# Kernel optimization log

Hardware: AMD Instinct MI355X
Metric: run time of the kernel (lower is better)

Reference implementation:

```python
import jax, jax.numpy as jnp
import numpy as np

T = 1_000_000          # number of t_eval points (~1 year at 30 s)
N_ROOMS = 10
N = 12                 # 2 latent wall nodes + n_rooms
DT = 30.0              # seconds between t_eval points
LOAD_SCALE = 50.0      # physical_cooling_scaling: W/m^2 scale for sigmoid(loads)


def setup_inputs() -> dict:
    key = jax.random.key(0)
    k1, k2, k3, k4, k5 = jax.random.split(key, 5)
    t_eval = jnp.arange(T, dtype=jnp.float32) * DT
    x0 = 26.0 * jnp.ones((N,), jnp.float32)  # reset_iv: 26 C at every node
    # Stable slow RC dynamics: negative-definite-ish A with small coupling
    A = (-1e-5 * jnp.eye(N, dtype=jnp.float32)
         + 1e-6 * jax.random.normal(k1, (N, N), jnp.float32))
    B = 1e-6 * jax.random.normal(k2, (N, 1 + N_ROOMS), jnp.float32)
    Tout_data = 10.0 + 20.0 * jax.random.uniform(k3, (T,), jnp.float32)  # outdoor temp samples on t_eval grid
    loads_raw = jax.random.normal(k4, (2, N_ROOMS), jnp.float32)         # pre-sigmoid [cool; gain] loads
    room_areas = 10.0 + 40.0 * jax.random.uniform(k5, (N_ROOMS,), jnp.float32)
    return {"t_eval": t_eval, "x0": x0, "A": A, "B": B,
            "Tout_data": Tout_data, "loads_raw": loads_raw, "room_areas": room_areas}


def reference(t_eval, x0, A, B, Tout_data, loads_raw, room_areas):
    # transform + physical scaling of loads (self.transform = sigmoid)
    loads = jax.nn.sigmoid(loads_raw) * LOAD_SCALE
    cool_load, gain_load = loads[0], loads[1]
    action = 0.0  # no cooling policy -> self.action stays 0
    Q_area = -cool_load * action + gain_load            # [n_rooms]
    Q_watts = Q_area * room_areas                        # proportional_heating
    # u = [Tout; Q_watts] so B@u = B[:,0]*Tout + B[:,1:]@Q_watts (Q constant over t)
    b0 = B[:, 0]                                         # [N]
    Bq = B[:, 1:] @ Q_watts                              # [N], constant forcing
    h = t_eval[1] - t_eval[0]                            # uniform step
    # Linear interp of Tout: value at t_i, midpoint t_i+h/2, and t_{i+1}
    To_t = Tout_data[:-1]
    To_n = Tout_data[1:]
    To_m = 0.5 * (To_t + To_n)

    def f(x, To):  # dy/dt = A x + B u
        return A @ x + b0 * To + Bq

    def step(x, tou):
        to_t, to_m, to_n = tou
        k1 = f(x, to_t)
        k2 = f(x + 0.5 * h * k1, to_m)
        k3 = f(x + 0.5 * h * k2, to_m)
        k4 = f(x + h * k3, to_n)
        xn = x + (h / 6.0) * (k1 + 2.0 * k2 + 2.0 * k3 + k4)
        return xn, xn

    _, xs = jax.lax.scan(step, x0, (To_t, To_m, To_n))
    return jnp.concatenate([x0[None, :], xs], axis=0)  # [T, N]
```

## Files before the change

kernel.cpp:

```cpp
#include <hip/hip_runtime.h>
#include <math.h>


#define S_STEPS 999999
#define CH      8
#define BLK     256
#define NB      489
#define NCHUNK  125000
#define LASTFULL 124998

#define OFF_M   0
#define OFF_C   144
#define OFF_AL  156
#define OFF_BE  168
#define OFF_K   192
#define OFF_P2  320
#define OFF_PA  1472
#define OFF_PL  1616
#define OFF_PD  2048
#define OFF_AGG 3200

#define FMA4(Q,a,b,c,d,acc) fmaf((Q).w,(d),fmaf((Q).z,(c),fmaf((Q).y,(b),fmaf((Q).x,(a),(acc)))))

__device__ __forceinline__ void mv_acc(const float* Pf, const float* x, float* y) {
  const float4* P = reinterpret_cast<const float4*>(Pf);
#pragma unroll
  for (int i = 0; i < 12; ++i) {
    float4 a = P[3*i], b = P[3*i+1], c = P[3*i+2];
    y[i] = FMA4(c, x[8],x[9],x[10],x[11],
            FMA4(b, x[4],x[5],x[6],x[7],
             FMA4(a, x[0],x[1],x[2],x[3], y[i])));
  }
}

__device__ __forceinline__ float rowdot(const float* Prow, const float* xv) {
  const float4* P = reinterpret_cast<const float4*>(Prow);
  float4 a = P[0], b = P[1], c = P[2];
  return FMA4(c, xv[8],xv[9],xv[10],xv[11],
          FMA4(b, xv[4],xv[5],xv[6],xv[7],
           FMA4(a, xv[0],xv[1],xv[2],xv[3], 0.f)));
}

__device__ __forceinline__ void fold_chunk(const float* __restrict__ cons,
                                           const float* tos, float* v) {
  const float4* Kq = reinterpret_cast<const float4*>(cons + OFF_K);
  float4 c0=Kq[0], c1=Kq[1], c2=Kq[2];
  v[0]=c0.x; v[1]=c0.y; v[2]=c0.z; v[3]=c0.w;
  v[4]=c1.x; v[5]=c1.y; v[6]=c1.z; v[7]=c1.w;
  v[8]=c2.x; v[9]=c2.y; v[10]=c2.z; v[11]=c2.w;
#pragma unroll
  for (int s = 0; s < 9; ++s) {
    float ts = tos[s];
    float4 ka=Kq[3*(s+1)], kb=Kq[3*(s+1)+1], kc=Kq[3*(s+1)+2];
    v[0]=fmaf(ka.x,ts,v[0]); v[1]=fmaf(ka.y,ts,v[1]); v[2]=fmaf(ka.z,ts,v[2]); v[3]=fmaf(ka.w,ts,v[3]);
    v[4]=fmaf(kb.x,ts,v[4]); v[5]=fmaf(kb.y,ts,v[5]); v[6]=fmaf(kb.z,ts,v[6]); v[7]=fmaf(kb.w,ts,v[7]);
    v[8]=fmaf(kc.x,ts,v[8]); v[9]=fmaf(kc.y,ts,v[9]); v[10]=fmaf(kc.z,ts,v[10]); v[11]=fmaf(kc.w,ts,v[11]);
  }
}

__global__ void __launch_bounds__(512) setup_kernel(
    const float* __restrict__ t_eval, const float* __restrict__ A,
    const float* __restrict__ Bm, const float* __restrict__ loads_raw,
    const float* __restrict__ areas, float* ws) {
  __shared__ double H1[144], H2[144], H3[144], H4[144], Md[144];
  __shared__ double Qa[144], Qb[144];
  __shared__ double C512s[144], C1024s[144], C2048s[144], C4096s[144];
  __shared__ double C8192s[144], C16384s[144], C32768s[144], Pd3s[144];
  __shared__ double cd[12], ald[12], bed[12], b0d[12], bqd[12];
  __shared__ double Vv[3][12], Kd[120];
  int t = threadIdx.x;
  double h = (double)t_eval[1] - (double)t_eval[0];
  if (t < 144) H1[t] = h * (double)A[t];
  if (t < 12) {
    b0d[t] = (double)Bm[t*11];
    double s = 0.0;
    for (int r = 0; r < 10; ++r) {
      double gq = 50.0 / (1.0 + exp(-(double)loads_raw[10 + r]));
      s += (double)Bm[t*11 + 1 + r] * (gq * (double)areas[r]);
    }
    bqd[t] = s;
  }
  if (t < 120) Kd[t] = 0.0;
  __syncthreads();
  if (t < 144) {
    int i=t/12, j=t%12; double s=0.0;
#pragma unroll
    for (int m = 0; m < 12; ++m) s += H1[i*12+m]*H1[m*12+j];
    H2[t]=s;
  }
  __syncthreads();
  if (t < 288) {
    int w=t/144, e=t%144, i=e/12, j=e%12;
    const double* Bp = w ? H2 : H1;
    double s = 0.0;
#pragma unroll
    for (int m = 0; m < 12; ++m) s += H2[i*12+m]*Bp[m*12+j];
    (w ? H4 : H3)[e] = s;
  }
  __syncthreads();
  if (t < 12) {
    double hb=0,h2b=0,h3b=0,hb0=0,h2b0=0,h3b0=0;
#pragma unroll
    for (int m = 0; m < 12; ++m) {
      hb  += H1[t*12+m]*bqd[m]; h2b  += H2[t*12+m]*bqd[m]; h3b  += H3[t*12+m]*bqd[m];
      hb0 += H1[t*12+m]*b0d[m]; h2b0 += H2[t*12+m]*b0d[m]; h3b0 += H3[t*12+m]*b0d[m];
    }
    double h6 = h / 6.0;
    cd[t]  = h6*(6.0*bqd[t] + 3.0*hb + h2b + 0.25*h3b);
    ald[t] = h6*(3.0*b0d[t] + 2.0*hb0 + 0.75*h2b0 + 0.25*h3b0);
    bed[t] = h6*(3.0*b0d[t] + hb0 + 0.25*h2b0);
    Vv[0][t]=ald[t]; Vv[1][t]=bed[t]; Vv[2][t]=cd[t];
    Kd[96+t] += ald[t]; Kd[108+t] += bed[t]; Kd[t] += cd[t];
  }
  if (t >= 144 && t < 288) {
    int e=t-144, i=e/12, j=e%12;
    Md[e] = (i==j ? 1.0 : 0.0) + H1[e] + 0.5*H2[e] + H3[e]/6.0 + H4[e]/24.0;
  }
  __syncthreads();
  if (t < 144) { ws[OFF_M+t] = (float)Md[t]; Qa[t] = Md[t]; }
  if (t < 12) {
    ws[OFF_C+t]=(float)cd[t]; ws[OFF_AL+t]=(float)ald[t]; ws[OFF_BE+t]=(float)bed[t];
  }
  __syncthreads();
  double* src = Qa; double* dst = Qb;
  for (int r = 1; r <= 15; ++r) {
    double acc = 0.0, ks = 0.0;
    if (t < 144) {
      int i=t/12, j=t%12;
#pragma unroll
      for (int m = 0; m < 12; ++m) acc += src[i*12+m]*src[m*12+j];
    }
    int w=0, i2=0;
    if (r <= 7 && t >= 256 && t < 292) {
      w=(t-256)/12; i2=(t-256)%12;
#pragma unroll
      for (int m = 0; m < 12; ++m) ks += Md[i2*12+m]*Vv[w][m];
    }
    __syncthreads();
    if (t < 144) {
      dst[t] = acc;
      if (r >= 3 && r <= 10) ws[OFF_P2+(r-3)*144+t] = (float)acc;
      if (r == 9)  C512s[t]=acc;
      if (r == 10) C1024s[t]=acc;
      if (r == 11) { C2048s[t]=acc;  ws[OFF_PL+t]       = (float)acc; }
      if (r == 12) { C4096s[t]=acc;  ws[OFF_PL+144+t]   = (float)acc; }
      if (r == 13) { C8192s[t]=acc;  ws[OFF_PD+144+t]   = (float)acc; }
      if (r == 14) { C16384s[t]=acc; ws[OFF_PD+2*144+t] = (float)acc; }
      if (r == 15) { C32768s[t]=acc; ws[OFF_PD+4*144+t] = (float)acc; }
    }
    if (r <= 7 && t >= 256 && t < 292) {
      Vv[w][i2] = ks;
      if (w == 0) Kd[(8-r)*12+i2] += ks;
      else if (w == 1) Kd[(9-r)*12+i2] += ks;
      else Kd[i2] += ks;
    }
    __syncthreads();
    double* tmp = src; src = dst; dst = tmp;
  }
  if (t < 120) ws[OFF_K+t] = (float)Kd[t];
  if (t < 144) ws[OFF_PD+t] = (t % 13 == 0) ? 1.f : 0.f;
  if (t < 432) {
    int w=t/144, e=t%144, i=e/12, j=e%12;
    const double* Ap = (w==0) ? C512s  : ((w==1) ? C2048s : C8192s);
    const double* Bp = (w==0) ? C1024s : ((w==1) ? C4096s : C16384s);
    double s = 0.0;
#pragma unroll
    for (int m = 0; m < 12; ++m) s += Ap[i*12+m]*Bp[m*12+j];
    if (w==0) ws[OFF_PA+e] = (float)s;
    else if (w==1) ws[OFF_PL+2*144+e] = (float)s;
    else { ws[OFF_PD+3*144+e] = (float)s; Pd3s[e] = s; }
  }
  __syncthreads();
  if (t < 432) {
    int w=t/144, e=t%144, i=e/12, j=e%12;
    const double* Ap = (w==0) ? C8192s : ((w==1) ? C16384s : Pd3s);
    double s = 0.0;
#pragma unroll
    for (int m = 0; m < 12; ++m) s += Ap[i*12+m]*C32768s[m*12+j];
    ws[OFF_PD+(5+w)*144+e] = (float)s;
  }
}

__global__ void __launch_bounds__(BLK, 2) block_agg(
    const float* __restrict__ cons, const float* __restrict__ To,
    const float* __restrict__ x0, float* __restrict__ agg) {
  __shared__ __align__(16) float Tw[48], Ta[24];
  int k = threadIdx.x, b = blockIdx.x;
  int g = b*BLK + k, base = g*CH;
  bool fullc = (g <= LASTFULL);
  float to_[9];
#pragma unroll
  for (int i = 0; i < 9; ++i) to_[i] = 0.f;
  if (fullc) {
    const float4* tp = reinterpret_cast<const float4*>(To + base);
    float4 ta = tp[0], tb = tp[1];
    to_[0]=ta.x; to_[1]=ta.y; to_[2]=ta.z; to_[3]=ta.w;
    to_[4]=tb.x; to_[5]=tb.y; to_[6]=tb.z; to_[7]=tb.w;
    to_[8]=To[base+8];
  }
  float v[12];
  if (fullc) fold_chunk(cons, to_, v);
  else {
#pragma unroll
    for (int i = 0; i < 12; ++i) v[i] = 0.f;
  }
  if (g == 0) {
    float xi[12];
#pragma unroll
    for (int i = 0; i < 12; ++i) xi[i] = x0[i];
    mv_acc(cons + OFF_P2, xi, v);
  }
  int j = k & 63;
#pragma unroll
  for (int l = 0; l < 6; ++l) {
    int off = 1 << l;
    float nb[12];
#pragma unroll
    for (int i = 0; i < 12; ++i) nb[i] = __shfl_up(v[i], (unsigned)off, 64);
    if (j >= off) mv_acc(cons + OFF_P2 + l*144, nb, v);
  }
  if (j == 63) {
#pragma unroll
    for (int i = 0; i < 12; ++i) Tw[(k>>6)*12 + i] = v[i];
  }
  __syncthreads();
  if (k < 24) {
    int p = k/12, comp = k - p*12;
    Ta[k] = rowdot(cons + OFF_P2 + 6*144 + comp*12, Tw + 2*p*12)
          + Tw[(2*p+1)*12 + comp];
  }
  __syncthreads();
  if (k < 12) {
    agg[b*12 + k] = rowdot(cons + OFF_P2 + 7*144 + k*12, Ta) + Ta[12 + k];
  }
}

__global__ void __launch_bounds__(BLK, 2) scan_expand(
    const float* __restrict__ cons, const float* __restrict__ To,
    const float* __restrict__ x0, const float* __restrict__ agg,
    float* __restrict__ out) {
  __shared__ __align__(16) float Tw[48];
  __shared__ __align__(16) float Pw[48];
  __shared__ __align__(16) float lkb[32*12];
  __shared__ __align__(16) float yv[8*12];
  __shared__ __align__(16) float zv[8*12];
  __shared__ __align__(16) float Xs[12];
  __shared__ __align__(16) float Qw[48];
  int k = threadIdx.x, b = blockIdx.x;
  int g = b*BLK + k, base = g*CH;
  bool active = (g < NCHUNK), fullc = (g <= LASTFULL);
  float to_[9];
#pragma unroll
  for (int i = 0; i < 9; ++i) to_[i] = 0.f;
  if (active) {
    const float4* tp = reinterpret_cast<const float4*>(To + base);
    float4 ta = tp[0], tb = tp[1];
    to_[0]=ta.x; to_[1]=ta.y; to_[2]=ta.z; to_[3]=ta.w;
    to_[4]=tb.x; to_[5]=tb.y; to_[6]=tb.z; to_[7]=tb.w;
    to_[8] = fullc ? To[base+8] : 0.f;
  }
  float v[12];
  if (fullc) fold_chunk(cons, to_, v);
  else {
#pragma unroll
    for (int i = 0; i < 12; ++i) v[i] = 0.f;
  }
  if (g == 0) {
    float xi[12];
#pragma unroll
    for (int i = 0; i < 12; ++i) xi[i] = x0[i];
    mv_acc(cons + OFF_P2, xi, v);
  }
  int j = k & 63, w = k >> 6;
#pragma unroll
  for (int l = 0; l < 6; ++l) {
    int off = 1 << l;
    float nb[12];
#pragma unroll
    for (int i = 0; i < 12; ++i) nb[i] = __shfl_up(v[i], (unsigned)off, 64);
    if (j >= off) mv_acc(cons + OFF_P2 + l*144, nb, v);
  }
  float se[12];
#pragma unroll
  for (int i = 0; i < 12; ++i) {
    float u = __shfl_up(v[i], 1u, 64);
    se[i] = (j == 0) ? 0.f : u;
  }
  if (j == 63) {
#pragma unroll
    for (int i = 0; i < 12; ++i) Tw[w*12 + i] = v[i];
  }
#pragma unroll
  for (int r = 0; r < 2; ++r) {
    int idx = k + r*BLK;
    if (idx < 384) {
      int slot = idx / 12, comp = idx - slot*12;
      int src = b - 1 - slot;
      float acc = 0.f;
      if (src >= 0) {
        int jj = slot & 3;
        const float* ag = agg + src*12;
        acc = (jj == 0) ? ag[comp]
            : rowdot(cons + OFF_PL + (jj-1)*144 + comp*12, ag);
      }
      lkb[idx] = acc;
    }
  }
  __syncthreads();
  if (k < 96) {
    int i = k/12, comp = k - i*12;
    yv[k] = lkb[(4*i)*12+comp] + lkb[(4*i+1)*12+comp]
          + lkb[(4*i+2)*12+comp] + lkb[(4*i+3)*12+comp];
  } else if (k >= 192 && k < 216) {
    int q = k - 192;
    if (q < 12) Pw[q] = 0.f;
    else Pw[q] = Tw[q-12];
  }
  __syncthreads();
  if (k < 96) {
    int i = k/12, comp = k - i*12;
    zv[k] = (i == 0) ? yv[comp]
          : rowdot(cons + OFF_PD + i*144 + comp*12, yv + i*12);
  } else if (k >= 192 && k < 204) {
    int comp = k - 192;
    Pw[24+comp] = rowdot(cons + OFF_P2 + 6*144 + comp*12, Pw+12) + Tw[12+comp];
  }
  __syncthreads();
  if (k < 12) {
    float s = 0.f;
#pragma unroll
    for (int i = 0; i < 8; ++i) s += zv[i*12 + k];
    Xs[k] = s;
  } else if (k >= 192 && k < 204) {
    int comp = k - 192;
    Pw[36+comp] = rowdot(cons + OFF_P2 + 6*144 + comp*12, Pw+24) + Tw[24+comp];
  }
  __syncthreads();
  if (k < 48) {
    int ww = k/12, comp = k - ww*12;
    float acc;
    if (ww == 0) acc = Xs[comp];
    else if (ww == 1) acc = rowdot(cons + OFF_P2 + 6*144 + comp*12, Xs);
    else if (ww == 2) acc = rowdot(cons + OFF_P2 + 7*144 + comp*12, Xs);
    else acc = rowdot(cons + OFF_PA + comp*12, Xs);
    Qw[k] = acc + Pw[k];
  }
  __syncthreads();
  if (!active) return;
  float x[12];
#pragma unroll
  for (int i = 0; i < 12; ++i) x[i] = Qw[w*12 + i];
#pragma unroll
  for (int l = 0; l < 6; ++l) {
    if ((j >> l) & 1) {
      float vn[12];
#pragma unroll
      for (int i = 0; i < 12; ++i) vn[i] = 0.f;
      mv_acc(cons + OFF_P2 + l*144, x, vn);
#pragma unroll
      for (int i = 0; i < 12; ++i) x[i] = vn[i];
    }
  }
#pragma unroll
  for (int i = 0; i < 12; ++i) x[i] += se[i];
  if (b == 0 && k == 0) {
#pragma unroll
    for (int i = 0; i < 12; ++i) x[i] += x0[i];
#pragma unroll
    for (int i = 0; i < 12; ++i) out[i] = x0[i];
  }
  float cv[12], av[12], bv[12];
#pragma unroll
  for (int i = 0; i < 12; ++i) {
    cv[i] = cons[OFF_C + i]; av[i] = cons[OFF_AL + i]; bv[i] = cons[OFF_BE + i];
  }
  const float4* Mq = reinterpret_cast<const float4*>(cons + OFF_M);
#pragma unroll
  for (int s = 0; s < CH; ++s) {
    float tot = to_[s], ton = to_[s+1];
    float xn[12];
#pragma unroll
    for (int i = 0; i < 12; ++i) {
      float4 a = Mq[3*i], bq = Mq[3*i+1], c = Mq[3*i+2];
      xn[i] = FMA4(c, x[8],x[9],x[10],x[11],
               FMA4(bq, x[4],x[5],x[6],x[7],
                FMA4(a, x[0],x[1],x[2],x[3],
                 fmaf(bv[i],ton,fmaf(av[i],tot,cv[i])))));
    }
    int tt = base + s;
    if (tt < S_STEPS) {
      float4* op = reinterpret_cast<float4*>(out + (size_t)(tt+1)*12);
      op[0] = make_float4(xn[0],xn[1],xn[2],xn[3]);
      op[1] = make_float4(xn[4],xn[5],xn[6],xn[7]);
      op[2] = make_float4(xn[8],xn[9],xn[10],xn[11]);
    }
#pragma unroll
    for (int i = 0; i < 12; ++i) x[i] = xn[i];
  }
}

extern "C" void kernel_launch(void* const* d_in, const int* in_sizes, int n_in,
                              void* d_out, int out_size, void* d_ws, size_t ws_size,
                              hipStream_t stream) {
  const float* t_eval    = (const float*)d_in[0];
  const float* x0        = (const float*)d_in[1];
  const float* A         = (const float*)d_in[2];
  const float* B         = (const float*)d_in[3];
  const float* To        = (const float*)d_in[4];
  const float* loads_raw = (const float*)d_in[5];
  const float* areas     = (const float*)d_in[6];
  float* out = (float*)d_out;
  float* ws  = (float*)d_ws;

  setup_kernel<<<1, 512, 0, stream>>>(t_eval, A, B, loads_raw, areas, ws);
  block_agg<<<NB, BLK, 0, stream>>>(ws, To, x0, ws + OFF_AGG);
  scan_expand<<<NB, BLK, 0, stream>>>(ws, To, x0, ws + OFF_AGG, out);
}
```

Measured before the change: 132.5 us.

## Fuse block aggregation and scan expansion into one cooperative kernel with grid sync

The per-block aggregate pass and the scan/expand pass become a single cooperative kernel. Each block computes its chunk fold and warp scan once, writes its aggregate, then waits at a grid-wide barrier before doing the lookback and expansion. This removes one kernel launch and the duplicated load of the To data and fold_chunk work. In exchange it adds a grid.sync, and it depends on all 489 blocks being co-resident, which the launch bounds of 2 blocks per CU are meant to allow.

Result: slower. 204.5 us (+54.4%).

```diff
diff --git a/kernel.cpp b/kernel.cpp
--- a/kernel.cpp
+++ b/kernel.cpp
@@ -1,5 +1,8 @@
 #include <hip/hip_runtime.h>
+#include <hip/hip_cooperative_groups.h>
 #include <math.h>
+
+namespace cg = cooperative_groups;
 
 
 #define S_STEPS 999999
@@ -181,71 +184,19 @@
   }
 }
 
-__global__ void __launch_bounds__(BLK, 2) block_agg(
+__global__ void __launch_bounds__(BLK, 2) fused_scan(
     const float* __restrict__ cons, const float* __restrict__ To,
-    const float* __restrict__ x0, float* __restrict__ agg) {
-  __shared__ __align__(16) float Tw[48], Ta[24];
-  int k = threadIdx.x, b = blockIdx.x;
-  int g = b*BLK + k, base = g*CH;
-  bool fullc = (g <= LASTFULL);
-  float to_[9];
-#pragma unroll
-  for (int i = 0; i < 9; ++i) to_[i] = 0.f;
-  if (fullc) {
-    const float4* tp = reinterpret_cast<const float4*>(To + base);
-    float4 ta = tp[0], tb = tp[1];
-    to_[0]=ta.x; to_[1]=ta.y; to_[2]=ta.z; to_[3]=ta.w;
-    to_[4]=tb.x; to_[5]=tb.y; to_[6]=tb.z; to_[7]=tb.w;
-    to_[8]=To[base+8];
-  }
-  float v[12];
-  if (fullc) fold_chunk(cons, to_, v);
-  else {
-#pragma unroll
-    for (int i = 0; i < 12; ++i) v[i] = 0.f;
-  }
-  if (g == 0) {
-    float xi[12];
-#pragma unroll
-    for (int i = 0; i < 12; ++i) xi[i] = x0[i];
-    mv_acc(cons + OFF_P2, xi, v);
-  }
-  int j = k & 63;
-#pragma unroll
-  for (int l = 0; l < 6; ++l) {
-    int off = 1 << l;
-    float nb[12];
-#pragma unroll
-    for (int i = 0; i < 12; ++i) nb[i] = __shfl_up(v[i], (unsigned)off, 64);
-    if (j >= off) mv_acc(cons + OFF_P2 + l*144, nb, v);
-  }
-  if (j == 63) {
-#pragma unroll
-    for (int i = 0; i < 12; ++i) Tw[(k>>6)*12 + i] = v[i];
-  }
-  __syncthreads();
-  if (k < 24) {
-    int p = k/12, comp = k - p*12;
-    Ta[k] = rowdot(cons + OFF_P2 + 6*144 + comp*12, Tw + 2*p*12)
-          + Tw[(2*p+1)*12 + comp];
-  }
-  __syncthreads();
-  if (k < 12) {
-    agg[b*12 + k] = rowdot(cons + OFF_P2 + 7*144 + k*12, Ta) + Ta[12 + k];
-  }
-}
-
-__global__ void __launch_bounds__(BLK, 2) scan_expand(
-    const float* __restrict__ cons, const float* __restrict__ To,
-    const float* __restrict__ x0, const float* __restrict__ agg,
+    const float* __restrict__ x0, float* __restrict__ agg,
     float* __restrict__ out) {
   __shared__ __align__(16) float Tw[48];
+  __shared__ __align__(16) float Ta[24];
   __shared__ __align__(16) float Pw[48];
   __shared__ __align__(16) float lkb[32*12];
   __shared__ __align__(16) float yv[8*12];
   __shared__ __align__(16) float zv[8*12];
   __shared__ __align__(16) float Xs[12];
   __shared__ __align__(16) float Qw[48];
+  cg::grid_group grid = cg::this_grid();
   int k = threadIdx.x, b = blockIdx.x;
   int g = b*BLK + k, base = g*CH;
   bool active = (g < NCHUNK), fullc = (g <= LASTFULL);
@@ -290,6 +241,18 @@
 #pragma unroll
     for (int i = 0; i < 12; ++i) Tw[w*12 + i] = v[i];
   }
+  __syncthreads();
+  if (k < 24) {
+    int p = k/12, comp = k - p*12;
+    Ta[k] = rowdot(cons + OFF_P2 + 6*144 + comp*12, Tw + 2*p*12)
+          + Tw[(2*p+1)*12 + comp];
+  }
+  __syncthreads();
+  if (k < 12) {
+    agg[b*12 + k] = rowdot(cons + OFF_P2 + 7*144 + k*12, Ta) + Ta[12 + k];
+  }
+  __threadfence();
+  grid.sync();
 #pragma unroll
   for (int r = 0; r < 2; ++r) {
     int idx = k + r*BLK;
@@ -413,6 +376,10 @@
   float* ws  = (float*)d_ws;
 
   setup_kernel<<<1, 512, 0, stream>>>(t_eval, A, B, loads_raw, areas, ws);
-  block_agg<<<NB, BLK, 0, stream>>>(ws, To, x0, ws + OFF_AGG);
-  scan_expand<<<NB, BLK, 0, stream>>>(ws, To, x0, ws + OFF_AGG, out);
-}
+
+  const float* cons = ws;
+  float* aggp = ws + OFF_AGG;
+  void* args[] = { (void*)&cons, (void*)&To, (void*)&x0, (void*)&aggp, (void*)&out };
+  hipLaunchCooperativeKernel((const void*)fused_scan, dim3(NB), dim3(BLK),
+                             args, 0, stream);
+}
```
